# Optimization experiments

Measured on AMD Instinct MI355X. Metric: run time of the kernel, lower is better.

## Reference

```python
import jax, jax.numpy as jnp
import numpy as np

B, S, H = 128, 512, 256
STEP = 1


def setup_inputs() -> dict:
    key = jax.random.key(0)
    ks = jax.random.split(key, 16)
    stdv = 1.0 / np.sqrt(H)
    u = lambda k, shape: jax.random.uniform(k, shape, jnp.float32, -stdv, stdv)
    return {
        "A": jax.random.uniform(ks[0], (B, S, 2 * S), jnp.float32),
        "hidden": jax.random.normal(ks[1], (B, S, H), jnp.float32),
        "mask": jnp.ones((B, S), jnp.int32),
        # linear_edge_in / linear_edge_out (Linear(H, H, bias=True))
        "W_in": u(ks[2], (H, H)),  "b_in": u(ks[3], (H,)),
        "W_out": u(ks[4], (H, H)), "b_out": u(ks[5], (H,)),
        # adjacency biases
        "b_iah": u(ks[6], (H,)), "b_oah": u(ks[7], (H,)),
        # GRU-style gate weights: w_ih [3H, 2H], w_hh [3H, H]
        "w_ih": u(ks[8], (3 * H, 2 * H)), "b_ih": u(ks[9], (3 * H,)),
        "w_hh": u(ks[10], (3 * H, H)),    "b_hh": u(ks[11], (3 * H,)),
    }


def _gnn_cell(A, hidden, W_in, b_in, W_out, b_out, b_iah, b_oah,
              w_ih, b_ih, w_hh, b_hh):
    s = hidden.shape[1]
    # edge-transformed features (torch F.linear: x @ W.T + b)
    h_in = jnp.einsum('bsh,gh->bsg', hidden, W_in) + b_in
    h_out = jnp.einsum('bsh,gh->bsg', hidden, W_out) + b_out
    # adjacency message passing: [B,S,S] @ [B,S,H]
    input_in = jnp.einsum('bij,bjh->bih', A[:, :, :s], h_in) + b_iah
    input_out = jnp.einsum('bij,bjh->bih', A[:, :, s:2 * s], h_out) + b_oah
    inputs = jnp.concatenate([input_in, input_out], axis=2)  # [B,S,2H]
    gi = jnp.einsum('bsi,gi->bsg', inputs, w_ih) + b_ih      # [B,S,3H]
    gh = jnp.einsum('bsh,gh->bsg', hidden, w_hh) + b_hh      # [B,S,3H]
    i_r, i_i, i_n = jnp.split(gi, 3, axis=2)
    h_r, h_i, h_n = jnp.split(gh, 3, axis=2)
    resetgate = jax.nn.sigmoid(i_r + h_r)
    inputgate = jax.nn.sigmoid(i_i + h_i)
    newgate = jnp.tanh(i_n + resetgate * h_n)
    return hidden + inputgate * (newgate - hidden)


def reference(A, hidden, mask, W_in, b_in, W_out, b_out, b_iah, b_oah,
              w_ih, b_ih, w_hh, b_hh):
    # GNN.forward with issrgnn=True: run GNNCell `step` times (mask unused)
    for _ in range(STEP):
        hidden = _gnn_cell(A, hidden, W_in, b_in, W_out, b_out,
                           b_iah, b_oah, w_ih, b_ih, w_hh, b_hh)
    return hidden
```

## Files before the change

kernel.cpp:

```cpp
#include <hip/hip_runtime.h>

#define B_ 128
#define S_ 512
#define H_ 256
#define M_ (B_*S_)

typedef __attribute__((ext_vector_type(4))) float f32x4;
typedef __attribute__((ext_vector_type(8))) short s16x8;
typedef __attribute__((ext_vector_type(4))) unsigned short u16x4;
typedef unsigned short ushort_t;

typedef __attribute__((address_space(1))) void as1_void;
typedef __attribute__((address_space(3))) void as3_void;

__device__ __forceinline__ unsigned short f2h(float f) {
  _Float16 h = (_Float16)f;
  return __builtin_bit_cast(unsigned short, h);
}
__device__ __forceinline__ float h2f(ushort_t u) {
  return (float)__builtin_bit_cast(_Float16, u);
}

__device__ __forceinline__ f32x4 mfma16(s16x8 a, s16x8 b, f32x4 c) {
  asm("v_mfma_f32_16x16x32_f16 %0, %1, %2, %0" : "+v"(c) : "v"(a), "v"(b));
  return c;
}

__device__ __forceinline__ void cp16(const void* g, void* l) {
  __builtin_amdgcn_global_load_lds((as1_void*)g, (as3_void*)l, 16, 0, 0);
}

__device__ __forceinline__ void waitvm(int n) {
  switch (n) {
    case 0:  asm volatile("s_waitcnt vmcnt(0)"  ::: "memory"); break;
    case 3:  asm volatile("s_waitcnt vmcnt(3)"  ::: "memory"); break;
    case 4:  asm volatile("s_waitcnt vmcnt(4)"  ::: "memory"); break;
    case 6:  asm volatile("s_waitcnt vmcnt(6)"  ::: "memory"); break;
    case 8:  asm volatile("s_waitcnt vmcnt(8)"  ::: "memory"); break;
    case 12: asm volatile("s_waitcnt vmcnt(12)" ::: "memory"); break;
  }
}

__device__ __forceinline__ int stage_kc(int lane) {
  return (lane & 3) ^ ((lane >> 3) & 3);
}
__device__ __forceinline__ int frag_off(int s, int lane) {
  int ln = lane & 15, kg = lane >> 4;
  return s * 512 + (ln * 4 + (kg ^ ((ln >> 1) & 3))) * 8;
}

__global__ void k_cvt_all(const float* __restrict__ hidden, ushort_t* __restrict__ hidh,
                          const float* __restrict__ W_in,  const float* __restrict__ W_out,
                          ushort_t* __restrict__ wcat,
                          const float* __restrict__ w_ih, ushort_t* __restrict__ wihh,
                          const float* __restrict__ w_hh, ushort_t* __restrict__ whhh) {
  int blk = blockIdx.x;
  const float* src; ushort_t* dst; int base;
  if (blk < 8192)      { src = hidden; dst = hidh;           base = blk; }
  else if (blk < 8224) { src = W_in;   dst = wcat;           base = blk - 8192; }
  else if (blk < 8256) { src = W_out;  dst = wcat + 65536;   base = blk - 8224; }
  else if (blk < 8448) { src = w_ih;   dst = wihh;           base = blk - 8256; }
  else                 { src = w_hh;   dst = whhh;           base = blk - 8448; }
  int i = base * 256 + threadIdx.x;
  const float* p = src + (size_t)i * 8;
  f32x4 a = *(const f32x4*)p;
  f32x4 b = *(const f32x4*)(p + 4);
  s16x8 o;
  o[0]=(short)f2h(a[0]); o[1]=(short)f2h(a[1]); o[2]=(short)f2h(a[2]); o[3]=(short)f2h(a[3]);
  o[4]=(short)f2h(b[0]); o[5]=(short)f2h(b[1]); o[6]=(short)f2h(b[2]); o[7]=(short)f2h(b[3]);
  *(s16x8*)(dst + (size_t)i * 8) = o;
}

__global__ __launch_bounds__(256, 2)
void k_gemm1(const ushort_t* __restrict__ hid, const ushort_t* __restrict__ wcat,
             const float* __restrict__ b_in, const float* __restrict__ b_out,
             ushort_t* __restrict__ hcatT) {
  __shared__ __attribute__((aligned(16))) ushort_t lA[3][8*512];
  __shared__ __attribute__((aligned(16))) ushort_t lB[3][16*512];
  const int flat = blockIdx.y * 8 + blockIdx.x;
  const int orig = (flat & 7) * 128 + (flat >> 3);
  const int bx = orig & 7, bb = orig >> 3;
  const int j0 = (bx >> 1) * 128;
  const int n0 = (bx & 1) * 256;
  const int tid = threadIdx.x;
  const int w = tid >> 6, lane = tid & 63;
  const int ln = lane & 15, kg = lane >> 4;
  const int wm = w >> 1, wn = w & 1;
  const int srow = lane >> 2, skc = stage_kc(lane);

  f32x4 acc[4][8];
  #pragma unroll
  for (int i = 0; i < 4; ++i)
    #pragma unroll
    for (int j = 0; j < 8; ++j) acc[i][j] = (f32x4){0.f,0.f,0.f,0.f};

  const size_t arow0 = (size_t)bb * 512 + j0;

  auto stage = [&](int t, int bsel) {
    int k0 = t * 32;
    #pragma unroll
    for (int it = 0; it < 2; ++it) {
      int s = it*4 + w;
      cp16(hid + (arow0 + s*16 + srow)*256 + k0 + skc*8, &lA[bsel][s*512]);
    }
    #pragma unroll
    for (int it = 0; it < 4; ++it) {
      int s = it*4 + w;
      cp16(wcat + (size_t)(n0 + s*16 + srow)*256 + k0 + skc*8, &lB[bsel][s*512]);
    }
  };
  auto compute = [&](int cur) {
    s16x8 af[4];
    #pragma unroll
    for (int mf = 0; mf < 4; ++mf)
      af[mf] = *(const s16x8*)&lA[cur][frag_off(wm*4 + mf, lane)];
    __builtin_amdgcn_s_setprio(1);
    #pragma unroll
    for (int nf = 0; nf < 8; ++nf) {
      s16x8 bf = *(const s16x8*)&lB[cur][frag_off(wn*8 + nf, lane)];
      #pragma unroll
      for (int mf = 0; mf < 4; ++mf) acc[mf][nf] = mfma16(af[mf], bf, acc[mf][nf]);
    }
    __builtin_amdgcn_s_setprio(0);
  };

  stage(0, 0); stage(1, 1);
  for (int t = 0; t < 6; ++t) {
    waitvm(6);
    __builtin_amdgcn_s_barrier();
    stage(t + 2, (t + 2) % 3);
    compute(t % 3);
  }
  waitvm(6); __builtin_amdgcn_s_barrier(); compute(6 % 3);
  waitvm(0); __builtin_amdgcn_s_barrier(); compute(7 % 3);

  #pragma unroll
  for (int nf = 0; nf < 8; ++nf) {
    int gn = n0 + wn*128 + nf*16 + ln;
    float bias = (gn < 256) ? b_in[gn] : b_out[gn - 256];
    #pragma unroll
    for (int mf = 0; mf < 4; ++mf) {
      int j = j0 + wm*64 + mf*16 + kg*4;
      u16x4 v;
      #pragma unroll
      for (int r = 0; r < 4; ++r) v[r] = f2h(acc[mf][nf][r] + bias);
      *(u16x4*)&hcatT[((size_t)(bb*512 + gn))*512 + j] = v;
    }
  }
}

__global__ __launch_bounds__(256, 2)
void k_gemm2(const float* __restrict__ A, const ushort_t* __restrict__ hcatT,
             const float* __restrict__ b_iah, const float* __restrict__ b_oah,
             ushort_t* __restrict__ inp) {
  __shared__ __attribute__((aligned(16))) ushort_t lA[2][8*512];
  __shared__ __attribute__((aligned(16))) ushort_t lB[3][16*512];
  const int flat = blockIdx.y * 8 + blockIdx.x;
  const int orig = (flat & 7) * 128 + (flat >> 3);
  const int bx = orig & 7, bb = orig >> 3;
  const int i0 = (bx >> 1) * 128;
  const int half = bx & 1;
  const int n0 = half * 256;
  const int tid = threadIdx.x;
  const int w = tid >> 6, lane = tid & 63;
  const int ln = lane & 15, kg = lane >> 4;
  const int wm = w >> 1, wn = w & 1;
  const int srow = lane >> 2, skc = stage_kc(lane);

  f32x4 acc[4][8];
  #pragma unroll
  for (int i = 0; i < 4; ++i)
    #pragma unroll
    for (int j = 0; j < 8; ++j) acc[i][j] = (f32x4){0.f,0.f,0.f,0.f};

  const float* Abase = A + ((size_t)bb*512 + i0)*1024 + half*512;
  f32x4 ra[2][4];

  auto loadA = [&](int t, f32x4 (&r)[4]) {
    int k0 = t * 32;
    #pragma unroll
    for (int it = 0; it < 2; ++it) {
      int s = it*4 + w;
      const float* p = Abase + (size_t)(s*16 + srow)*1024 + k0 + skc*8;
      r[it*2]   = *(const f32x4*)p;
      r[it*2+1] = *(const f32x4*)(p + 4);
    }
  };
  auto stageB = [&](int t, int bsel) {
    int k0 = t * 32;
    #pragma unroll
    for (int it = 0; it < 4; ++it) {
      int s = it*4 + w;
      cp16(hcatT + ((size_t)(bb*512 + n0 + s*16 + srow))*512 + k0 + skc*8, &lB[bsel][s*512]);
    }
  };
  auto writeA = [&](const f32x4 (&r)[4], int bsel) {
    #pragma unroll
    for (int it = 0; it < 2; ++it) {
      int s = it*4 + w;
      s16x8 o;
      o[0]=(short)f2h(r[it*2][0]); o[1]=(short)f2h(r[it*2][1]);
      o[2]=(short)f2h(r[it*2][2]); o[3]=(short)f2h(r[it*2][3]);
      o[4]=(short)f2h(r[it*2+1][0]); o[5]=(short)f2h(r[it*2+1][1]);
      o[6]=(short)f2h(r[it*2+1][2]); o[7]=(short)f2h(r[it*2+1][3]);
      *(s16x8*)&lA[bsel][s*512 + lane*8] = o;
    }
  };
  auto compute = [&](int acur, int bcur) {
    s16x8 af[4];
    #pragma unroll
    for (int mf = 0; mf < 4; ++mf)
      af[mf] = *(const s16x8*)&lA[acur][frag_off(wm*4 + mf, lane)];
    __builtin_amdgcn_s_setprio(1);
    #pragma unroll
    for (int nf = 0; nf < 8; ++nf) {
      s16x8 bf = *(const s16x8*)&lB[bcur][frag_off(wn*8 + nf, lane)];
      #pragma unroll
      for (int mf = 0; mf < 4; ++mf) acc[mf][nf] = mfma16(af[mf], bf, acc[mf][nf]);
    }
    __builtin_amdgcn_s_setprio(0);
  };

  loadA(0, ra[0]); stageB(0, 0);
  loadA(1, ra[1]); stageB(1, 1);
  waitvm(12);
  writeA(ra[0], 0);
  asm volatile("s_waitcnt lgkmcnt(0)" ::: "memory");

  #pragma unroll
  for (int t = 0; t < 16; ++t) {
    waitvm(t < 15 ? 8 : 0);
    __builtin_amdgcn_s_barrier();
    if (t + 2 < 16) { loadA(t + 2, ra[t & 1]); stageB(t + 2, (t + 2) % 3); }
    compute(t & 1, t % 3);
    if (t + 1 < 16) {
      waitvm(t + 2 < 16 ? 12 : 4);
      writeA(ra[(t + 1) & 1], (t + 1) & 1);
      asm volatile("s_waitcnt lgkmcnt(0)" ::: "memory");
    }
  }

  #pragma unroll
  for (int nf = 0; nf < 8; ++nf) {
    int gn = n0 + wn*128 + nf*16 + ln;
    float bias = half ? b_oah[gn - 256] : b_iah[gn];
    #pragma unroll
    for (int mf = 0; mf < 4; ++mf) {
      #pragma unroll
      for (int r = 0; r < 4; ++r) {
        int i = i0 + wm*64 + mf*16 + kg*4 + r;
        inp[((size_t)(bb*512 + i))*512 + gn] = f2h(acc[mf][nf][r] + bias);
      }
    }
  }
}

__global__ __launch_bounds__(256, 2)
void k_gemm3(const ushort_t* __restrict__ inp, const ushort_t* __restrict__ hidh,
             const ushort_t* __restrict__ wih, const ushort_t* __restrict__ whh,
             const float* __restrict__ b_ih, const float* __restrict__ b_hh,
             float* __restrict__ out) {
  __shared__ __attribute__((aligned(16))) ushort_t lIn[4][8*512];
  __shared__ __attribute__((aligned(16))) ushort_t lW[4][6*512];
  const int flat = blockIdx.y * 8 + blockIdx.x;
  const int orig = (flat & 7) * 512 + (flat >> 3);
  const int h0 = (orig & 7) * 32;
  const int m0 = (orig >> 3) * 128;
  const int tid = threadIdx.x;
  const int w = tid >> 6, lane = tid & 63;
  const int ln = lane & 15, kg = lane >> 4;
  const int wm2 = w >> 1, wh = w & 1;
  const int srow = lane >> 2, skc = stage_kc(lane);

  f32x4 aR[4], aI[4], aIN[4], aHN[4];
  #pragma unroll
  for (int m = 0; m < 4; ++m) {
    aR[m] = (f32x4){0.f,0.f,0.f,0.f}; aI[m] = (f32x4){0.f,0.f,0.f,0.f};
    aIN[m] = (f32x4){0.f,0.f,0.f,0.f}; aHN[m] = (f32x4){0.f,0.f,0.f,0.f};
  }

  auto stage = [&](int gs, int bsel) {
    if (gs < 16) {
      int k0 = gs * 32;
      #pragma unroll
      for (int it = 0; it < 2; ++it) {
        int s = it*4 + w;
        cp16(inp + (size_t)(m0 + s*16 + srow)*512 + k0 + skc*8, &lIn[bsel][s*512]);
      }
      #pragma unroll
      for (int it = 0; it < 2; ++it) {
        int s = it*4 + w;
        if (s < 6) {
          int g = s >> 1, hh = (s & 1)*16 + srow;
          cp16(wih + (size_t)(g*256 + h0 + hh)*512 + k0 + skc*8, &lW[bsel][s*512]);
        }
      }
    } else {
      int k0 = (gs - 16) * 32;
      #pragma unroll
      for (int it = 0; it < 2; ++it) {
        int s = it*4 + w;
        cp16(hidh + (size_t)(m0 + s*16 + srow)*256 + k0 + skc*8, &lIn[bsel][s*512]);
      }
      #pragma unroll
      for (int it = 0; it < 2; ++it) {
        int s = it*4 + w;
        if (s < 6) {
          int g = s >> 1, hh = (s & 1)*16 + srow;
          cp16(whh + (size_t)(g*256 + h0 + hh)*256 + k0 + skc*8, &lW[bsel][s*512]);
        }
      }
    }
  };

  auto compute = [&](int cur, f32x4 (&aN)[4]) {
    s16x8 af[4];
    #pragma unroll
    for (int mf = 0; mf < 4; ++mf)
      af[mf] = *(const s16x8*)&lIn[cur][frag_off(wm2*4 + mf, lane)];
    __builtin_amdgcn_s_setprio(1);
    #pragma unroll
    for (int g = 0; g < 3; ++g) {
      s16x8 bf = *(const s16x8*)&lW[cur][frag_off(g*2 + wh, lane)];
      #pragma unroll
      for (int mf = 0; mf < 4; ++mf) {
        f32x4& a = (g == 0 ? aR[mf] : g == 1 ? aI[mf] : aN[mf]);
        a = mfma16(af[mf], bf, a);
      }
    }
    __builtin_amdgcn_s_setprio(0);
  };

  stage(0, 0); stage(1, 1); stage(2, 2);
  for (int t = 0; t < 16; ++t) {
    if (w < 2) waitvm(8); else waitvm(6);
    __builtin_amdgcn_s_barrier();
    stage(t + 3, (t + 3) & 3);
    compute(t & 3, aIN);
  }
  for (int t = 16; t < 21; ++t) {
    if (w < 2) waitvm(8); else waitvm(6);
    __builtin_amdgcn_s_barrier();
    stage(t + 3, (t + 3) & 3);
    compute(t & 3, aHN);
  }
  if (w < 2) waitvm(8); else waitvm(6);
  __builtin_amdgcn_s_barrier(); compute(21 & 3, aHN);
  if (w < 2) waitvm(4); else waitvm(3);
  __builtin_amdgcn_s_barrier(); compute(22 & 3, aHN);
  waitvm(0);
  __builtin_amdgcn_s_barrier(); compute(23 & 3, aHN);

  {
    int h = h0 + wh*16 + ln;
    float br  = b_ih[h]       + b_hh[h];
    float bi  = b_ih[256 + h] + b_hh[256 + h];
    float bni = b_ih[512 + h];
    float bnh = b_hh[512 + h];
    #pragma unroll
    for (int mf = 0; mf < 4; ++mf) {
      #pragma unroll
      for (int r = 0; r < 4; ++r) {
        int m = m0 + wm2*64 + mf*16 + kg*4 + r;
        float rg = 1.0f / (1.0f + __expf(-(aR[mf][r] + br)));
        float ig = 1.0f / (1.0f + __expf(-(aI[mf][r] + bi)));
        float narg = aIN[mf][r] + bni + rg * (aHN[mf][r] + bnh);
        float e2 = __expf(2.0f * narg);
        float ng = 1.0f - 2.0f / (e2 + 1.0f);
        float hv = h2f(hidh[(size_t)m*256 + h]);
        out[(size_t)m*256 + h] = hv + ig * (ng - hv);
      }
    }
  }
}

extern "C" void kernel_launch(void* const* d_in, const int* in_sizes, int n_in,
                              void* d_out, int out_size, void* d_ws, size_t ws_size,
                              hipStream_t stream) {
  const float* A      = (const float*)d_in[0];
  const float* hidden = (const float*)d_in[1];
  const float* W_in   = (const float*)d_in[3];
  const float* b_in   = (const float*)d_in[4];
  const float* W_out  = (const float*)d_in[5];
  const float* b_out  = (const float*)d_in[6];
  const float* b_iah  = (const float*)d_in[7];
  const float* b_oah  = (const float*)d_in[8];
  const float* w_ih   = (const float*)d_in[9];
  const float* b_ih   = (const float*)d_in[10];
  const float* w_hh   = (const float*)d_in[11];
  const float* b_hh   = (const float*)d_in[12];
  float* out = (float*)d_out;

  char* ws = (char*)d_ws;
  ushort_t* hidh  = (ushort_t*)(ws);
  ushort_t* wcat  = (ushort_t*)(ws + 33554432);
  ushort_t* wihh  = (ushort_t*)(ws + 33816576);
  ushort_t* whhh  = (ushort_t*)(ws + 34603008);
  ushort_t* hcatT = (ushort_t*)(ws + 34996224);
  ushort_t* inp   = (ushort_t*)(ws + 102105088);

  k_cvt_all<<<8544, 256, 0, stream>>>(hidden, hidh, W_in, W_out, wcat,
                                      w_ih, wihh, w_hh, whhh);

  k_gemm1<<<dim3(8, 128), 256, 0, stream>>>(hidh, wcat, b_in, b_out, hcatT);
  k_gemm2<<<dim3(8, 128), 256, 0, stream>>>(A, hcatT, b_iah, b_oah, inp);
  k_gemm3<<<dim3(8, 512), 256, 0, stream>>>(inp, hidh, wihh, whhh, b_ih, b_hh, out);
}
```

Measured before the change: 299.8 us.

## Rewrite gate GEMM as single-wave blocks loading fragments directly from global

The gate GEMM kernel drops its LDS-staged, 4-wave, 4-buffer async pipeline. It becomes one 64-thread wave per block computing a 64x16 tile per gate, with MFMA fragments loaded straight from global memory into registers and double-buffered one step ahead. This removes LDS traffic and barriers. In exchange, each block reuses far less data (tile shrinks from 128x32 to 64x16), so global/L2 traffic rises, and the direct loads are uncoalesced 16-byte fragment reads.

```diff
diff --git a/kernel.cpp b/kernel.cpp
--- a/kernel.cpp
+++ b/kernel.cpp
@@ -33,7 +33,6 @@
 __device__ __forceinline__ void waitvm(int n) {
   switch (n) {
     case 0:  asm volatile("s_waitcnt vmcnt(0)"  ::: "memory"); break;
-    case 3:  asm volatile("s_waitcnt vmcnt(3)"  ::: "memory"); break;
     case 4:  asm volatile("s_waitcnt vmcnt(4)"  ::: "memory"); break;
     case 6:  asm volatile("s_waitcnt vmcnt(6)"  ::: "memory"); break;
     case 8:  asm volatile("s_waitcnt vmcnt(8)"  ::: "memory"); break;
@@ -255,22 +254,17 @@
   }
 }
 
-__global__ __launch_bounds__(256, 2)
+__global__ __launch_bounds__(64, 3)
 void k_gemm3(const ushort_t* __restrict__ inp, const ushort_t* __restrict__ hidh,
              const ushort_t* __restrict__ wih, const ushort_t* __restrict__ whh,
              const float* __restrict__ b_ih, const float* __restrict__ b_hh,
              float* __restrict__ out) {
-  __shared__ __attribute__((aligned(16))) ushort_t lIn[4][8*512];
-  __shared__ __attribute__((aligned(16))) ushort_t lW[4][6*512];
-  const int flat = blockIdx.y * 8 + blockIdx.x;
-  const int orig = (flat & 7) * 512 + (flat >> 3);
-  const int h0 = (orig & 7) * 32;
-  const int m0 = (orig >> 3) * 128;
-  const int tid = threadIdx.x;
-  const int w = tid >> 6, lane = tid & 63;
+  const int flat = blockIdx.x;
+  const int orig = (flat & 7) * 2048 + (flat >> 3);
+  const int h0 = (orig & 15) * 16;
+  const int m0 = (orig >> 4) * 64;
+  const int lane = threadIdx.x;
   const int ln = lane & 15, kg = lane >> 4;
-  const int wm2 = w >> 1, wh = w & 1;
-  const int srow = lane >> 2, skc = stage_kc(lane);
 
   f32x4 aR[4], aI[4], aIN[4], aHN[4];
   #pragma unroll
@@ -279,80 +273,56 @@
     aIN[m] = (f32x4){0.f,0.f,0.f,0.f}; aHN[m] = (f32x4){0.f,0.f,0.f,0.f};
   }
 
-  auto stage = [&](int gs, int bsel) {
-    if (gs < 16) {
-      int k0 = gs * 32;
-      #pragma unroll
-      for (int it = 0; it < 2; ++it) {
-        int s = it*4 + w;
-        cp16(inp + (size_t)(m0 + s*16 + srow)*512 + k0 + skc*8, &lIn[bsel][s*512]);
-      }
-      #pragma unroll
-      for (int it = 0; it < 2; ++it) {
-        int s = it*4 + w;
-        if (s < 6) {
-          int g = s >> 1, hh = (s & 1)*16 + srow;
-          cp16(wih + (size_t)(g*256 + h0 + hh)*512 + k0 + skc*8, &lW[bsel][s*512]);
-        }
-      }
+  const ushort_t* pAgi = inp  + (size_t)(m0 + ln)*512 + kg*8;
+  const ushort_t* pBgi = wih  + (size_t)(h0 + ln)*512 + kg*8;
+  const ushort_t* pAgh = hidh + (size_t)(m0 + ln)*256 + kg*8;
+  const ushort_t* pBgh = whh  + (size_t)(h0 + ln)*256 + kg*8;
+
+  auto loadfrags = [&](int t, s16x8 (&fa)[4], s16x8 (&fb)[3]) {
+    if (t < 16) {
+      int k0 = t * 32;
+      #pragma unroll
+      for (int mf = 0; mf < 4; ++mf)
+        fa[mf] = *(const s16x8*)(pAgi + (size_t)mf*16*512 + k0);
+      #pragma unroll
+      for (int g = 0; g < 3; ++g)
+        fb[g] = *(const s16x8*)(pBgi + (size_t)g*256*512 + k0);
     } else {
-      int k0 = (gs - 16) * 32;
-      #pragma unroll
-      for (int it = 0; it < 2; ++it) {
-        int s = it*4 + w;
-        cp16(hidh + (size_t)(m0 + s*16 + srow)*256 + k0 + skc*8, &lIn[bsel][s*512]);
-      }
-      #pragma unroll
-      for (int it = 0; it < 2; ++it) {
-        int s = it*4 + w;
-        if (s < 6) {
-          int g = s >> 1, hh = (s & 1)*16 + srow;
-          cp16(whh + (size_t)(g*256 + h0 + hh)*256 + k0 + skc*8, &lW[bsel][s*512]);
-        }
-      }
-    }
-  };
-
-  auto compute = [&](int cur, f32x4 (&aN)[4]) {
-    s16x8 af[4];
-    #pragma unroll
-    for (int mf = 0; mf < 4; ++mf)
-      af[mf] = *(const s16x8*)&lIn[cur][frag_off(wm2*4 + mf, lane)];
+      int k0 = (t - 16) * 32;
+      #pragma unroll
+      for (int mf = 0; mf < 4; ++mf)
+        fa[mf] = *(const s16x8*)(pAgh + (size_t)mf*16*256 + k0);
+      #pragma unroll
+      for (int g = 0; g < 3; ++g)
+        fb[g] = *(const s16x8*)(pBgh + (size_t)g*256*256 + k0);
+    }
+  };
+
+  s16x8 cA[4], cB[3];
+  loadfrags(0, cA, cB);
+  #pragma unroll
+  for (int t = 0; t < 24; ++t) {
+    s16x8 nA[4], nB[3];
+    if (t + 1 < 24) loadfrags(t + 1, nA, nB);
     __builtin_amdgcn_s_setprio(1);
     #pragma unroll
-    for (int g = 0; g < 3; ++g) {
-      s16x8 bf = *(const s16x8*)&lW[cur][frag_off(g*2 + wh, lane)];
-      #pragma unroll
-      for (int mf = 0; mf < 4; ++mf) {
-        f32x4& a = (g == 0 ? aR[mf] : g == 1 ? aI[mf] : aN[mf]);
-        a = mfma16(af[mf], bf, a);
-      }
+    for (int mf = 0; mf < 4; ++mf) {
+      aR[mf] = mfma16(cA[mf], cB[0], aR[mf]);
+      aI[mf] = mfma16(cA[mf], cB[1], aI[mf]);
+      if (t < 16) aIN[mf] = mfma16(cA[mf], cB[2], aIN[mf]);
+      else        aHN[mf] = mfma16(cA[mf], cB[2], aHN[mf]);
     }
     __builtin_amdgcn_s_setprio(0);
-  };
-
-  stage(0, 0); stage(1, 1); stage(2, 2);
-  for (int t = 0; t < 16; ++t) {
-    if (w < 2) waitvm(8); else waitvm(6);
-    __builtin_amdgcn_s_barrier();
-    stage(t + 3, (t + 3) & 3);
-    compute(t & 3, aIN);
-  }
-  for (int t = 16; t < 21; ++t) {
-    if (w < 2) waitvm(8); else waitvm(6);
-    __builtin_amdgcn_s_barrier();
-    stage(t + 3, (t + 3) & 3);
-    compute(t & 3, aHN);
-  }
-  if (w < 2) waitvm(8); else waitvm(6);
-  __builtin_amdgcn_s_barrier(); compute(21 & 3, aHN);
-  if (w < 2) waitvm(4); else waitvm(3);
-  __builtin_amdgcn_s_barrier(); compute(22 & 3, aHN);
-  waitvm(0);
-  __builtin_amdgcn_s_barrier(); compute(23 & 3, aHN);
+    if (t + 1 < 24) {
+      #pragma unroll
+      for (int i = 0; i < 4; ++i) cA[i] = nA[i];
+      #pragma unroll
+      for (int i = 0; i < 3; ++i) cB[i] = nB[i];
+    }
+  }
 
   {
-    int h = h0 + wh*16 + ln;
+    int h = h0 + ln;
     float br  = b_ih[h]       + b_hh[h];
     float bi  = b_ih[256 + h] + b_hh[256 + h];
     float bni = b_ih[512 + h];
@@ -361,7 +331,7 @@
     for (int mf = 0; mf < 4; ++mf) {
       #pragma unroll
       for (int r = 0; r < 4; ++r) {
-        int m = m0 + wm2*64 + mf*16 + kg*4 + r;
+        int m = m0 + mf*16 + kg*4 + r;
         float rg = 1.0f / (1.0f + __expf(-(aR[mf][r] + br)));
         float ig = 1.0f / (1.0f + __expf(-(aI[mf][r] + bi)));
         float narg = aIN[mf][r] + bni + rg * (aHN[mf][r] + bnh);
@@ -404,5 +374,5 @@
 
   k_gemm1<<<dim3(8, 128), 256, 0, stream>>>(hidh, wcat, b_in, b_out, hcatT);
   k_gemm2<<<dim3(8, 128), 256, 0, stream>>>(A, hcatT, b_iah, b_oah, inp);
-  k_gemm3<<<dim3(8, 512), 256, 0, stream>>>(inp, hidh, wihh, whhh, b_ih, b_hh, out);
-}
+  k_gemm3<<<16384, 64, 0, stream>>>(inp, hidh, wihh, whhh, b_ih, b_hh, out);
+}
```

New measurement: 452.1 us. 50.8% more time.
